# Optimization experiments

Hardware: AMD Instinct MI355X
Metric: run time of the kernel (lower is better)

## Reference

```python
import jax, jax.numpy as jnp
import numpy as np

jax.config.update("jax_enable_x64", True)

B = 16384          # batch size (rows of features)
K = 256            # num_unlabel (clusters)
EPS = 0.05         # sinkhorn epsilon
GAMMA = 5.0        # KL regularizer weight
LR = 0.1           # SGD lr for w
MOM = 0.99         # SGD momentum
N_INNER = 3        # sinkhorn iterations
N_OUTER = 10       # outer optimization iterations


def setup_inputs() -> dict:
    key = jax.random.key(0)
    features = jax.random.normal(key, (B, K), dtype=jnp.float32)
    w = jnp.ones((1, K), dtype=jnp.float32) / K  # torch Parameter init: ones/K
    return {"features": features, "w": w, "head": 0}


def _sinkhorn(logits, w):
    """SinkhornKnopp_im.forward: logits [B,K] -> Q [B,K] (float64), preds=logits64."""
    logits64 = logits.astype(jnp.float64)
    Q = jnp.exp(logits64 / EPS).T            # [K, B]
    Q = Q / jnp.sum(Q)
    K2 = jax.nn.softmax(w, axis=1).astype(jnp.float64)  # [1, K] marginal prior
    Bn = Q.shape[1]
    for _ in range(N_INNER):
        Q = Q / jnp.sum(Q, axis=1, keepdims=True)       # row normalize
        Q = Q * K2.T                                    # scale rows by prior
        Q = Q / jnp.sum(Q, axis=0, keepdims=True)       # column normalize
        Q = Q / Bn
    Q = Q * Bn
    return Q.T, logits64                                # [B, K], [B, K]


def _total_loss(w, features):
    Q, preds = _sinkhorn(features, w)
    loss = -jnp.mean(jnp.sum(Q * preds, axis=1))
    # KLDivLoss(batchmean): input = log_softmax(w).T [K,1], target = softmax(w0).T = 1/K
    logw = jax.nn.log_softmax(w, axis=1)[0]             # [K]
    t = jnp.float32(1.0 / K)
    reg = jnp.sum(t * (jnp.log(t) - logw)) / K
    return loss + GAMMA * reg.astype(jnp.float64), Q


def reference(features, w, head):
    features = jax.lax.stop_gradient(features)  # features.detach()

    def step(carry, _):
        w, buf, _ = carry
        (_, Q), g = jax.value_and_grad(_total_loss, has_aux=True)(w, features)
        # clip_grad_norm_(params, 1)
        norm = jnp.sqrt(jnp.sum(g.astype(jnp.float64) ** 2)).astype(g.dtype)
        g = g * jnp.minimum(jnp.float32(1.0), jnp.float32(1.0) / (norm + 1e-6))
        # SGD with momentum 0.99 (buf starts at 0 -> first buf = g, matching torch)
        buf = MOM * buf + g
        w = w - LR * buf
        return (w, buf, Q), None

    Q0 = jnp.zeros((features.shape[0], K), dtype=jnp.float64)
    (w_f, buf_f, Q), _ = jax.lax.scan(
        step, (w, jnp.zeros_like(w), Q0), None, length=N_OUTER
    )
    return Q  # Q from the last outer iteration (computed with pre-update w)
```

## Files before the change

kernel.cpp:

```cpp
#include <hip/hip_runtime.h>


namespace {

constexpr int KDIM = 256;
constexpr int NBLK = 256;
constexpr int ROWS = 64;
constexpr int NRED = 16;
constexpr int NREP = 16;
constexpr int NPH  = 48;
constexpr float L2E20 = 28.853900817779268f;

constexpr size_t RES_OFF = 2ull * NBLK * KDIM;
constexpr size_t WS_DBL  = RES_OFF + (size_t)NPH * NREP * KDIM;

__device__ __forceinline__ double fast_exp_d(double x) {
  const double LOG2E  = 1.4426950408889634074;
  const double LN2_HI = 6.93147180369123816490e-01;
  const double LN2_LO = 1.90821492927058770002e-10;
  double n = rint(x * LOG2E);
  double t = fma(-n, LN2_HI, x);
  t = fma(-n, LN2_LO, t);
  double p = 2.4801587301587302e-05;
  p = fma(p, t, 1.9841269841269841e-04);
  p = fma(p, t, 1.3888888888888889e-03);
  p = fma(p, t, 8.3333333333333333e-03);
  p = fma(p, t, 4.1666666666666664e-02);
  p = fma(p, t, 1.6666666666666666e-01);
  p = fma(p, t, 0.5);
  p = fma(p, t, 1.0);
  p = fma(p, t, 1.0);
  long long ni = (long long)n;
  double s = __longlong_as_double((unsigned long long)(ni + 1023LL) << 52);
  return p * s;
}

__device__ __forceinline__ double wave_sum_d(double v) {
#pragma unroll
  for (int o = 32; o > 0; o >>= 1) v += __shfl_down(v, o);
  return v;
}
__device__ __forceinline__ double wave_max_d(double v) {
#pragma unroll
  for (int o = 32; o > 0; o >>= 1) v = fmax(v, __shfl_down(v, o));
  return v;
}

__device__ __forceinline__ double pload(const double* p) {
  return __hip_atomic_load(p, __ATOMIC_RELAXED, __HIP_MEMORY_SCOPE_AGENT);
}
__device__ __forceinline__ void pstore(double* p, double v) {
  __hip_atomic_store(p, v, __ATOMIC_RELAXED, __HIP_MEMORY_SCOPE_AGENT);
}

}

__global__ __launch_bounds__(256) void kInitWS(double* __restrict__ ws) {
  const double QN = __builtin_nan("");
  size_t gid = (size_t)blockIdx.x * 256 + threadIdx.x;
  size_t stride = (size_t)gridDim.x * 256;
  for (size_t j = gid; j < WS_DBL; j += stride) ws[j] = QN;
}

__global__ __launch_bounds__(256, 1) void sink_main(
    const float* __restrict__ feat, const float* __restrict__ w_in,
    float* __restrict__ out, double* __restrict__ ws) {
  __shared__ float  Et[ROWS * KDIM];
  __shared__ float  Ft[ROWS * KDIM];
  __shared__ double alpha[KDIM];
  __shared__ double tmp1[KDIM];
  __shared__ double sfin[16];
  __shared__ double v1s[ROWS], v2s[ROWS], v3s[ROWS];
  __shared__ double grow[ROWS], wrow[ROWS], sbr[ROWS];
  __shared__ float  mrow[ROWS];
  __shared__ double sred[8];

  const int t = threadIdx.x, bid = blockIdx.x;
  const int wv = t >> 6, lane = t & 63;
  const int b0 = bid * ROWS;
  const double QN = __builtin_nan("");

  double* P   = ws;
  double* res = ws + RES_OFF;

  auto blk_sum = [&](double v) -> double {
    v = wave_sum_d(v);
    __syncthreads();
    if (lane == 0) sred[wv] = v;
    __syncthreads();
    return sred[0] + sred[1] + sred[2] + sred[3];
  };
  auto blk_max = [&](double v) -> double {
    v = wave_max_d(v);
    __syncthreads();
    if (lane == 0) sred[wv + 4] = v;
    __syncthreads();
    return fmax(fmax(sred[4], sred[5]), fmax(sred[6], sred[7]));
  };

  auto allreduce = [&](unsigned ph, double pa) -> double {
    const int par = (int)(ph & 1);
    double* Pp = P + (size_t)par * NBLK * KDIM;
    double* R  = res + (size_t)ph * NREP * KDIM;
    pstore(Pp + (size_t)bid * KDIM + t, pa);
    if (bid < NRED) {
      const int kl = t & 15, seg = t >> 4;
      const int k = bid * 16 + kl;
      double* base = Pp + (size_t)(seg * 16) * KDIM + k;
      double v[16];
#pragma unroll
      for (int j = 0; j < 16; ++j) v[j] = pload(base + (size_t)j * KDIM);
      for (;;) {
        bool again = false;
#pragma unroll
        for (int j = 0; j < 16; ++j)
          if (__builtin_isnan(v[j])) {
            v[j] = pload(base + (size_t)j * KDIM);
            if (__builtin_isnan(v[j])) again = true;
          }
        if (!again) break;
        __builtin_amdgcn_s_sleep(1);
      }
      double a = 0.0;
#pragma unroll
      for (int j = 0; j < 16; ++j) a += v[j];
#pragma unroll
      for (int j = 0; j < 16; ++j) pstore(base + (size_t)j * KDIM, QN);
      asm volatile("s_waitcnt vmcnt(0)" ::: "memory");
      tmp1[t] = a;
      __syncthreads();
      if (t < 16) {
        double s = 0.0;
#pragma unroll
        for (int sg = 0; sg < 16; ++sg) s += tmp1[sg * 16 + t];
        sfin[t] = s;
      }
      __syncthreads();
      pstore(R + (size_t)seg * KDIM + k, sfin[kl]);
    }
    const double* re = R + (size_t)(bid & (NREP - 1)) * KDIM + t;
    double r = pload(re);
    while (__builtin_isnan(r)) {
      __builtin_amdgcn_s_sleep(1);
      r = pload(re);
    }
    return r;
  };

  auto row_pass = [&](double* dstv) {
    double a0 = alpha[4 * lane + 0], a1 = alpha[4 * lane + 1];
    double a2 = alpha[4 * lane + 2], a3 = alpha[4 * lane + 3];
#pragma unroll 4
    for (int r = wv; r < ROWS; r += 4) {
      float4 e4 = ((const float4*)(Et + r * KDIM))[lane];
      double s1 = a0 * (double)e4.x + a1 * (double)e4.y +
                  a2 * (double)e4.z + a3 * (double)e4.w;
      s1 = wave_sum_d(s1);
      if (lane == 0) dstv[r] = s1;
    }
  };
  auto col_partial = [&]() -> double {
    double a = 0.0;
#pragma unroll 8
    for (int r = 0; r < ROWS; ++r) a += (double)Et[r * KDIM + t] * wrow[r];
    return a;
  };

  {
    const float4* src = (const float4*)(feat + (size_t)b0 * KDIM);
    float4* dst = (float4*)Ft;
#pragma unroll
    for (int s = 0; s < 16; ++s) dst[s * 256 + t] = src[s * 256 + t];
  }
  __syncthreads();
  for (int r = wv; r < ROWS; r += 4) {
    float4 f4 = ((const float4*)(Ft + r * KDIM))[lane];
    float m = fmaxf(fmaxf(f4.x, f4.y), fmaxf(f4.z, f4.w));
#pragma unroll
    for (int o = 32; o > 0; o >>= 1) m = fmaxf(m, __shfl_down(m, o));
    if (lane == 0) {
      mrow[r] = m;
      sbr[r] = fast_exp_d(20.0 * (double)m);
    }
  }
  __syncthreads();
  double pu0 = 0.0;
#pragma unroll 8
  for (int r = 0; r < ROWS; ++r) {
    float e = exp2f((Ft[r * KDIM + t] - mrow[r]) * L2E20);
    Et[r * KDIM + t] = e;
    pu0 += (double)e * sbr[r];
  }
  float w_t = w_in[t], buf_t = 0.0f;
  double k2_t;
  {
    double x = (double)w_t;
    double m = blk_max(x);
    double e = fast_exp_d(x - m);
    double s = blk_sum(e);
    k2_t = e / s;
  }
  unsigned ph = 0;
  double u0_t = allreduce(ph, pu0);

  for (int it = 0; it < 10; ++it) {
    double u1_t, u2_t;

    alpha[t] = k2_t / u0_t;
    __syncthreads();
    row_pass(v1s);
    __syncthreads();
    if (t < ROWS) wrow[t] = 1.0 / (16384.0 * v1s[t]);
    __syncthreads();
    {
      double pa = col_partial();
      ++ph; u1_t = allreduce(ph, pa);
    }

    alpha[t] = k2_t / u1_t;
    __syncthreads();
    row_pass(v2s);
    __syncthreads();
    if (t < ROWS) wrow[t] = 1.0 / (16384.0 * v2s[t]);
    __syncthreads();
    {
      double pa = col_partial();
      ++ph; u2_t = allreduce(ph, pa);
    }

    if (it == 9) {
      alpha[t] = k2_t / u2_t;
      __syncthreads();
      row_pass(v3s);
      __syncthreads();
      if (t < ROWS) wrow[t] = 1.0 / v3s[t];
      __syncthreads();
      double a3 = alpha[t];
#pragma unroll 4
      for (int r = 0; r < ROWS; ++r)
        out[(size_t)(b0 + r) * KDIM + t] =
            (float)(a3 * (double)Et[r * KDIM + t] * wrow[r]);
      return;
    }

    alpha[t] = k2_t / u2_t;
    __syncthreads();
    {
      double a0 = alpha[4 * lane + 0], a1 = alpha[4 * lane + 1];
      double a2 = alpha[4 * lane + 2], a3 = alpha[4 * lane + 3];
#pragma unroll 2
      for (int r = wv; r < ROWS; r += 4) {
        float4 e4 = ((const float4*)(Et + r * KDIM))[lane];
        float4 f4 = ((const float4*)(Ft + r * KDIM))[lane];
        double p0 = a0 * (double)e4.x, p1 = a1 * (double)e4.y;
        double p2 = a2 * (double)e4.z, p3 = a3 * (double)e4.w;
        double s1 = p0 + p1 + p2 + p3;
        double s2 = p0 * (double)f4.x + p1 * (double)f4.y +
                    p2 * (double)f4.z + p3 * (double)f4.w;
        s1 = wave_sum_d(s1);
        s2 = wave_sum_d(s2);
        if (lane == 0) {
          v3s[r] = s1;
          grow[r] = s2 / (16384.0 * s1 * s1);
        }
      }
    }
    __syncthreads();
    if (t < ROWS) wrow[t] = -1.0 / (16384.0 * v3s[t]);
    __syncthreads();
    double gsum_t;
    {
      double ac1 = 0.0, ac2 = 0.0;
#pragma unroll 8
      for (int r = 0; r < ROWS; ++r) {
        double ed = (double)Et[r * KDIM + t];
        ac1 += ed * (double)Ft[r * KDIM + t] * wrow[r];
        ac2 += ed * grow[r];
      }
      ++ph; gsum_t = allreduce(ph, ac1 + ac2);
    }

    alpha[t] = -gsum_t * k2_t / (u2_t * u2_t);
    __syncthreads();
    row_pass(grow);
    __syncthreads();
    if (t < ROWS) wrow[t] = -grow[t] / (16384.0 * v2s[t] * v2s[t]);
    __syncthreads();
    double ga2_t;
    {
      double pa = col_partial();
      ++ph; ga2_t = allreduce(ph, pa);
    }

    alpha[t] = -ga2_t * k2_t / (u1_t * u1_t);
    __syncthreads();
    row_pass(grow);
    __syncthreads();
    if (t < ROWS) wrow[t] = -grow[t] / (16384.0 * v1s[t] * v1s[t]);
    __syncthreads();
    double ga1_t;
    {
      double pa = col_partial();
      ++ph; ga1_t = allreduce(ph, pa);
    }

    {
      double gk2 = gsum_t / u2_t + ga2_t / u1_t + ga1_t / u0_t;
      double dot = blk_sum(k2_t * gk2);
      double gw = k2_t * (gk2 - dot) + 5.0 * (k2_t / 256.0 - 1.0 / 65536.0);
      double n2 = blk_sum(gw * gw);
      float normf = (float)sqrt(n2);
      float sc = fminf(1.0f, 1.0f / (normf + 1e-6f));
      float g = (float)gw * sc;
      buf_t = 0.99f * buf_t + g;
      w_t = w_t - 0.1f * buf_t;
      double x = (double)w_t;
      double m = blk_max(x);
      double e = fast_exp_d(x - m);
      double s = blk_sum(e);
      k2_t = e / s;
    }
  }
}

extern "C" void kernel_launch(void* const* d_in, const int* in_sizes, int n_in,
                              void* d_out, int out_size, void* d_ws,
                              size_t ws_size, hipStream_t stream) {
  (void)in_sizes; (void)n_in; (void)out_size; (void)ws_size;
  const float* feat = (const float*)d_in[0];
  const float* w_in = (const float*)d_in[1];
  float* out = (float*)d_out;
  double* ws = (double*)d_ws;

  kInitWS<<<128, 256, 0, stream>>>(ws);
  sink_main<<<NBLK, 256, 0, stream>>>(feat, w_in, out, ws);
}
```

Before: 638.6 us.

## Replace NaN-sentinel polling with monotonic phase flags in grid allreduce

The cross-block allreduce now signals readiness with per-block monotonic phase counters instead of poisoning the partial buffers with NaN and spinning on each value. Reducer blocks wait on 256 flags, then read the partials once. Results go to a double-buffered slot, and a second flag array tells consumers when it is ready. This cuts the large NaN initialization kernel down to clearing about 288 flags and removes the re-poison stores. In exchange it adds extra waitcnt and __syncthreads barriers per phase, and it relies on relaxed atomics plus vmcnt waits for ordering.

```diff
diff --git a/kernel.cpp b/kernel.cpp
--- a/kernel.cpp
+++ b/kernel.cpp
@@ -8,11 +8,11 @@
 constexpr int ROWS = 64;
 constexpr int NRED = 16;
 constexpr int NREP = 16;
-constexpr int NPH  = 48;
 constexpr float L2E20 = 28.853900817779268f;
 
 constexpr size_t RES_OFF = 2ull * NBLK * KDIM;
-constexpr size_t WS_DBL  = RES_OFF + (size_t)NPH * NREP * KDIM;
+constexpr size_t FLG_OFF = RES_OFF + 2ull * NREP * KDIM;
+constexpr size_t WS_DBL  = FLG_OFF + 64;
 
 __device__ __forceinline__ double fast_exp_d(double x) {
   const double LOG2E  = 1.4426950408889634074;
@@ -52,14 +52,19 @@
 __device__ __forceinline__ void pstore(double* p, double v) {
   __hip_atomic_store(p, v, __ATOMIC_RELAXED, __HIP_MEMORY_SCOPE_AGENT);
 }
+__device__ __forceinline__ unsigned aload(const unsigned* p) {
+  return __hip_atomic_load(p, __ATOMIC_RELAXED, __HIP_MEMORY_SCOPE_AGENT);
+}
+__device__ __forceinline__ void astore(unsigned* p, unsigned v) {
+  __hip_atomic_store(p, v, __ATOMIC_RELAXED, __HIP_MEMORY_SCOPE_AGENT);
+}
 
 }
 
 __global__ __launch_bounds__(256) void kInitWS(double* __restrict__ ws) {
-  const double QN = __builtin_nan("");
   size_t gid = (size_t)blockIdx.x * 256 + threadIdx.x;
-  size_t stride = (size_t)gridDim.x * 256;
-  for (size_t j = gid; j < WS_DBL; j += stride) ws[j] = QN;
+  unsigned* fl = (unsigned*)(ws + FLG_OFF);
+  if (gid < 272 + 16) fl[gid] = 0u;
 }
 
 __global__ __launch_bounds__(256, 1) void sink_main(
@@ -78,10 +83,11 @@
   const int t = threadIdx.x, bid = blockIdx.x;
   const int wv = t >> 6, lane = t & 63;
   const int b0 = bid * ROWS;
-  const double QN = __builtin_nan("");
-
-  double* P   = ws;
-  double* res = ws + RES_OFF;
+
+  double* P     = ws;
+  double* res   = ws + RES_OFF;
+  unsigned* flag1 = (unsigned*)(ws + FLG_OFF);
+  unsigned* flag2 = flag1 + 256;
 
   auto blk_sum = [&](double v) -> double {
     v = wave_sum_d(v);
@@ -101,32 +107,26 @@
   auto allreduce = [&](unsigned ph, double pa) -> double {
     const int par = (int)(ph & 1);
     double* Pp = P + (size_t)par * NBLK * KDIM;
-    double* R  = res + (size_t)ph * NREP * KDIM;
+    double* Rp = res + (size_t)par * NREP * KDIM;
     pstore(Pp + (size_t)bid * KDIM + t, pa);
+    asm volatile("s_waitcnt vmcnt(0)" ::: "memory");
+    __syncthreads();
+    if (t == 0) astore(flag1 + bid, ph);
     if (bid < NRED) {
+      {
+        unsigned v = aload(flag1 + t);
+        while (v < ph) {
+          __builtin_amdgcn_s_sleep(1);
+          v = aload(flag1 + t);
+        }
+      }
+      __syncthreads();
       const int kl = t & 15, seg = t >> 4;
       const int k = bid * 16 + kl;
-      double* base = Pp + (size_t)(seg * 16) * KDIM + k;
-      double v[16];
-#pragma unroll
-      for (int j = 0; j < 16; ++j) v[j] = pload(base + (size_t)j * KDIM);
-      for (;;) {
-        bool again = false;
-#pragma unroll
-        for (int j = 0; j < 16; ++j)
-          if (__builtin_isnan(v[j])) {
-            v[j] = pload(base + (size_t)j * KDIM);
-            if (__builtin_isnan(v[j])) again = true;
-          }
-        if (!again) break;
-        __builtin_amdgcn_s_sleep(1);
-      }
+      const double* base = Pp + (size_t)(seg * 16) * KDIM + k;
       double a = 0.0;
 #pragma unroll
-      for (int j = 0; j < 16; ++j) a += v[j];
-#pragma unroll
-      for (int j = 0; j < 16; ++j) pstore(base + (size_t)j * KDIM, QN);
-      asm volatile("s_waitcnt vmcnt(0)" ::: "memory");
+      for (int j = 0; j < 16; ++j) a += pload(base + (size_t)j * KDIM);
       tmp1[t] = a;
       __syncthreads();
       if (t < 16) {
@@ -136,15 +136,20 @@
         sfin[t] = s;
       }
       __syncthreads();
-      pstore(R + (size_t)seg * KDIM + k, sfin[kl]);
-    }
-    const double* re = R + (size_t)(bid & (NREP - 1)) * KDIM + t;
-    double r = pload(re);
-    while (__builtin_isnan(r)) {
-      __builtin_amdgcn_s_sleep(1);
-      r = pload(re);
-    }
-    return r;
+      pstore(Rp + (size_t)seg * KDIM + k, sfin[kl]);
+      asm volatile("s_waitcnt vmcnt(0)" ::: "memory");
+      __syncthreads();
+      if (t == 0) astore(flag2 + bid, ph);
+    }
+    if (t < NREP) {
+      unsigned v = aload(flag2 + t);
+      while (v < ph) {
+        __builtin_amdgcn_s_sleep(1);
+        v = aload(flag2 + t);
+      }
+    }
+    __syncthreads();
+    return pload(Rp + (size_t)(bid & (NREP - 1)) * KDIM + t);
   };
 
   auto row_pass = [&](double* dstv) {
@@ -200,7 +205,7 @@
     double s = blk_sum(e);
     k2_t = e / s;
   }
-  unsigned ph = 0;
+  unsigned ph = 1;
   double u0_t = allreduce(ph, pu0);
 
   for (int it = 0; it < 10; ++it) {
@@ -332,6 +337,6 @@
   float* out = (float*)d_out;
   double* ws = (double*)d_ws;
 
-  kInitWS<<<128, 256, 0, stream>>>(ws);
+  kInitWS<<<2, 256, 0, stream>>>(ws);
   sink_main<<<NBLK, 256, 0, stream>>>(feat, w_in, out, ws);
 }
```

After: 709.0 us. +11.0%, slower.
